# Kernel optimization log

Measured on AMD Instinct MI355X. Metric: run time of the kernel, lower is better.

Reference implementation:

```python
import jax, jax.numpy as jnp
import numpy as np

B, S, E, D, H, DH, FF, NL = 16384, 4, 1152, 192, 4, 48, 768, 2


def _ln(x, w, b, eps=1e-5):
    m = jnp.mean(x, axis=-1, keepdims=True)
    v = jnp.mean((x - m) ** 2, axis=-1, keepdims=True)
    return (x - m) * jax.lax.rsqrt(v + eps) * w + b


def _gelu(x):
    # torch nn.GELU / TransformerEncoderLayer(activation='gelu') use exact erf GELU
    return jax.nn.gelu(x, approximate=False)


def _pos_enc():
    pos = np.arange(S, dtype=np.float32)[:, None]
    div = np.exp(np.arange(0, D, 2, dtype=np.float32) * (-np.log(10000.0) / D))
    pe = np.zeros((S, D), dtype=np.float32)
    pe[:, 0::2] = np.sin(pos * div)
    pe[:, 1::2] = np.cos(pos * div)
    return jnp.asarray(pe)


def setup_inputs() -> dict:
    key = jax.random.key(0)
    ks = jax.random.split(key, 16)
    w = lambda k, shape: jax.random.normal(k, shape, jnp.float32) * 0.05
    return {
        'embeddings': jax.random.normal(ks[0], (B, S, E), jnp.float32),
        'in_ln_w': jnp.ones((E,), jnp.float32), 'in_ln_b': jnp.zeros((E,), jnp.float32),
        'in_proj_w': w(ks[1], (D, E)), 'in_proj_b': jnp.zeros((D,), jnp.float32),
        'qkv_w': w(ks[2], (NL, 3 * D, D)), 'qkv_b': jnp.zeros((NL, 3 * D), jnp.float32),
        'attn_out_w': w(ks[3], (NL, D, D)), 'attn_out_b': jnp.zeros((NL, D), jnp.float32),
        'ln1_w': jnp.ones((NL, D), jnp.float32), 'ln1_b': jnp.zeros((NL, D), jnp.float32),
        'ln2_w': jnp.ones((NL, D), jnp.float32), 'ln2_b': jnp.zeros((NL, D), jnp.float32),
        'ff1_w': w(ks[4], (NL, FF, D)), 'ff1_b': jnp.zeros((NL, FF), jnp.float32),
        'ff2_w': w(ks[5], (NL, D, FF)), 'ff2_b': jnp.zeros((NL, D), jnp.float32),
        'head_ln_w': jnp.ones((D,), jnp.float32), 'head_ln_b': jnp.zeros((D,), jnp.float32),
        'h1_w': w(ks[6], (256, D)), 'h1_b': jnp.zeros((256,), jnp.float32),
        'h2_w': w(ks[7], (64, 256)), 'h2_b': jnp.zeros((64,), jnp.float32),
        'h3_w': w(ks[8], (1, 64)) * 0.1, 'h3_b': jnp.zeros((1,), jnp.float32),
    }


def reference(embeddings, in_ln_w, in_ln_b, in_proj_w, in_proj_b,
              qkv_w, qkv_b, attn_out_w, attn_out_b,
              ln1_w, ln1_b, ln2_w, ln2_b,
              ff1_w, ff1_b, ff2_w, ff2_b,
              head_ln_w, head_ln_b, h1_w, h1_b, h2_w, h2_b, h3_w, h3_b):
    # input_proj: LN -> Linear(E, D) -> GELU (dropout is identity in eval)
    x = _ln(embeddings, in_ln_w, in_ln_b)
    x = _gelu(x @ in_proj_w.T + in_proj_b)
    # sinusoidal positional encoding
    x = x + _pos_enc()[None]
    scale = 1.0 / jnp.sqrt(jnp.float32(DH))
    # norm_first TransformerEncoder layers
    for i in range(NL):
        xn = _ln(x, ln1_w[i], ln1_b[i])
        qkv = xn @ qkv_w[i].T + qkv_b[i]                       # (B, S, 3D)
        q, k, v = jnp.split(qkv, 3, axis=-1)
        q = q.reshape(B, S, H, DH)
        k = k.reshape(B, S, H, DH)
        v = v.reshape(B, S, H, DH)
        scores = jnp.einsum('bqhd,bkhd->bhqk', q, k) * scale   # (B, H, S, S)
        attn = jax.nn.softmax(scores, axis=-1)
        o = jnp.einsum('bhqk,bkhd->bqhd', attn, v).reshape(B, S, D)
        x = x + (o @ attn_out_w[i].T + attn_out_b[i])
        xn = _ln(x, ln2_w[i], ln2_b[i])
        x = x + (_gelu(xn @ ff1_w[i].T + ff1_b[i]) @ ff2_w[i].T + ff2_b[i])
    pooled = x.mean(axis=1)                                    # (B, D)
    h = _ln(pooled, head_ln_w, head_ln_b)
    h = _gelu(h @ h1_w.T + h1_b)
    h = _gelu(h @ h2_w.T + h2_b)
    return (h @ h3_w.T + h3_b)[:, 0]                           # (B,)
```

## Files before the change

### kernel.cpp

```cpp
#include <hip/hip_runtime.h>
#include <hip/hip_bf16.h>
#include <math.h>

#define B_   16384
#define S_   4
#define E_   1152
#define D_   192
#define FF_  768
#define NL_  2
#define MTOK (B_ * S_)

typedef __attribute__((ext_vector_type(8))) _Float16 half8;
typedef __attribute__((ext_vector_type(4))) float floatx4;

__device__ __forceinline__ float gelu_f(float x) {
  return 0.5f * x * (1.0f + erff(x * 0.70710678118654752f));
}

__global__ __launch_bounds__(256) void cvt_f16_kernel(const float* __restrict__ s,
                                                      _Float16* __restrict__ d) {
  int i = (blockIdx.x * 256 + threadIdx.x) * 8;
  float4 a = *(const float4*)(s + i);
  float4 b = *(const float4*)(s + i + 4);
  half8 h;
  h[0] = (_Float16)a.x; h[1] = (_Float16)a.y; h[2] = (_Float16)a.z; h[3] = (_Float16)a.w;
  h[4] = (_Float16)b.x; h[5] = (_Float16)b.y; h[6] = (_Float16)b.z; h[7] = (_Float16)b.w;
  *(half8*)(d + i) = h;
}

__global__ __launch_bounds__(256) void prep_inproj_w(
    const float* __restrict__ W, const float* __restrict__ g,
    const float* __restrict__ b, const float* __restrict__ bias,
    _Float16* __restrict__ Wh, float* __restrict__ c1, float* __restrict__ c2) {
  const int n = blockIdx.x * 4 + (threadIdx.x >> 6);
  const int lane = threadIdx.x & 63;
  const float* Wr = W + (size_t)n * 1152;
  _Float16* Whr = Wh + (size_t)n * 1152;
  float s1 = 0.f, s2 = 0.f;
  #pragma unroll
  for (int j = 0; j < 18; ++j) {
    int k = lane + 64 * j;
    float wv = Wr[k];
    _Float16 h = (_Float16)(wv * g[k]);
    Whr[k] = h;
    s1 += (float)h;
    s2 = fmaf(b[k], wv, s2);
  }
  #pragma unroll
  for (int off = 1; off < 64; off <<= 1) {
    s1 += __shfl_xor(s1, off);
    s2 += __shfl_xor(s2, off);
  }
  if (lane == 0) { c1[n] = s1; c2[n] = s2 + bias[n]; }
}

__global__ __launch_bounds__(256) void inproj2_kernel(
    const float* __restrict__ emb, const _Float16* __restrict__ whp,
    const float* __restrict__ c1g, const float* __restrict__ c2g,
    float* __restrict__ xout, float* __restrict__ stD) {
  __shared__ __align__(16) _Float16 As[64][72];
  __shared__ float stats_[64][2];
  __shared__ float red_[4][64][2];
  __shared__ float pe_[4][192];
  const int tid = threadIdx.x;
  const int m0 = blockIdx.x * 64;
  const int w = tid >> 6, lane = tid & 63;
  const int ln16 = lane & 15, quad = lane >> 4;
  const int r_a = tid >> 2;
  const int c_a = (tid & 3) * 16;

  for (int i = tid; i < 768; i += 256) {
    int r = i / 192, col = i - r * 192;
    float ang = (float)r * expf((float)(col & ~1) * (-0.047970522770709292f));
    pe_[r][col] = (col & 1) ? cosf(ang) : sinf(ang);
  }

  const float* Arow = emb + (size_t)(m0 + r_a) * 1152 + c_a;
  const _Float16* wb = whp + (size_t)(w * 48 + ln16) * 1152 + quad * 8;

  float4 pa[4];
  auto loadA = [&](int k0) {
    #pragma unroll
    for (int j = 0; j < 4; ++j) pa[j] = *(const float4*)(Arow + k0 + j * 4);
  };

  float s = 0.f, q = 0.f;
  floatx4 acc[4][3] = {};
  loadA(0);
  for (int k0 = 0; k0 < 1152; k0 += 64) {
    __syncthreads();
    half8 h0, h1;
    h0[0] = (_Float16)pa[0].x; h0[1] = (_Float16)pa[0].y;
    h0[2] = (_Float16)pa[0].z; h0[3] = (_Float16)pa[0].w;
    h0[4] = (_Float16)pa[1].x; h0[5] = (_Float16)pa[1].y;
    h0[6] = (_Float16)pa[1].z; h0[7] = (_Float16)pa[1].w;
    h1[0] = (_Float16)pa[2].x; h1[1] = (_Float16)pa[2].y;
    h1[2] = (_Float16)pa[2].z; h1[3] = (_Float16)pa[2].w;
    h1[4] = (_Float16)pa[3].x; h1[5] = (_Float16)pa[3].y;
    h1[6] = (_Float16)pa[3].z; h1[7] = (_Float16)pa[3].w;
    *(half8*)&As[r_a][c_a] = h0;
    *(half8*)&As[r_a][c_a + 8] = h1;
    #pragma unroll
    for (int j = 0; j < 4; ++j) {
      s += pa[j].x + pa[j].y + pa[j].z + pa[j].w;
      q = fmaf(pa[j].x, pa[j].x, q); q = fmaf(pa[j].y, pa[j].y, q);
      q = fmaf(pa[j].z, pa[j].z, q); q = fmaf(pa[j].w, pa[j].w, q);
    }
    __syncthreads();
    if (k0 + 64 < 1152) loadA(k0 + 64);
    #pragma unroll
    for (int kk = 0; kk < 64; kk += 32) {
      half8 af[4], bf[3];
      #pragma unroll
      for (int mt = 0; mt < 4; ++mt)
        af[mt] = *(const half8*)&As[mt * 16 + ln16][kk + quad * 8];
      #pragma unroll
      for (int nt = 0; nt < 3; ++nt)
        bf[nt] = *(const half8*)(wb + (size_t)nt * 16 * 1152 + k0 + kk);
      #pragma unroll
      for (int mt = 0; mt < 4; ++mt)
        #pragma unroll
        for (int nt = 0; nt < 3; ++nt)
          acc[mt][nt] = __builtin_amdgcn_mfma_f32_16x16x32_f16(
              af[mt], bf[nt], acc[mt][nt], 0, 0, 0);
    }
  }

  s += __shfl_xor(s, 1); s += __shfl_xor(s, 2);
  q += __shfl_xor(q, 1); q += __shfl_xor(q, 2);
  if ((tid & 3) == 0) {
    float mean = s * (1.f / 1152.f);
    stats_[r_a][0] = mean;
    stats_[r_a][1] = rsqrtf(q * (1.f / 1152.f) - mean * mean + 1e-5f);
  }
  __syncthreads();

  float c1v[3], c2v[3];
  #pragma unroll
  for (int nt = 0; nt < 3; ++nt) {
    c1v[nt] = c1g[w * 48 + nt * 16 + ln16];
    c2v[nt] = c2g[w * 48 + nt * 16 + ln16];
  }
  float* xg = xout + (size_t)m0 * 192;
  #pragma unroll
  for (int mt = 0; mt < 4; ++mt) {
    #pragma unroll
    for (int r = 0; r < 4; ++r) {
      const int row = mt * 16 + quad * 4 + r;
      const float rm = stats_[row][0], rr = stats_[row][1];
      float so = 0.f, qo = 0.f;
      #pragma unroll
      for (int nt = 0; nt < 3; ++nt) {
        const int col = w * 48 + nt * 16 + ln16;
        float v = rr * (acc[mt][nt][r] - rm * c1v[nt]) + c2v[nt];
        v = gelu_f(v);
        v += pe_[r][col];
        xg[(size_t)row * 192 + col] = v;
        so += v;
        qo = fmaf(v, v, qo);
      }
      so += __shfl_xor(so, 1); so += __shfl_xor(so, 2);
      so += __shfl_xor(so, 4); so += __shfl_xor(so, 8);
      qo += __shfl_xor(qo, 1); qo += __shfl_xor(qo, 2);
      qo += __shfl_xor(qo, 4); qo += __shfl_xor(qo, 8);
      if (ln16 == 0) { red_[w][row][0] = so; red_[w][row][1] = qo; }
    }
  }
  __syncthreads();
  if (tid < 64) {
    float so = red_[0][tid][0] + red_[1][tid][0] + red_[2][tid][0] + red_[3][tid][0];
    float qo = red_[0][tid][1] + red_[1][tid][1] + red_[2][tid][1] + red_[3][tid][1];
    float mean = so * (1.f / 192.f);
    stD[2 * (m0 + tid)] = mean;
    stD[2 * (m0 + tid) + 1] = rsqrtf(qo * (1.f / 192.f) - mean * mean + 1e-5f);
  }
}

__global__ __launch_bounds__(256) void layer_attn_kernel(
    float* __restrict__ x, const _Float16* __restrict__ wqkv,
    const float* __restrict__ bqkv, const _Float16* __restrict__ wao,
    const float* __restrict__ bao, const float* __restrict__ ln1g,
    const float* __restrict__ ln1b_, float* __restrict__ stD) {
  __shared__ __align__(16) _Float16 xh[32][200];
  __shared__ __align__(16) _Float16 qk[32][584];
  __shared__ float sp[8][4][4][4];
  const int tid = threadIdx.x;
  const int m0 = blockIdx.x * 32;
  const int w = tid >> 6, lane = tid & 63;
  const int ln16 = lane & 15, quad = lane >> 4;

  {
    const int ra = tid >> 3, ca = (tid & 7) * 24;
    const float sm = stD[2 * (m0 + ra)], srs = stD[2 * (m0 + ra) + 1];
    const float* Ar = x + (size_t)(m0 + ra) * 192 + ca;
    #pragma unroll
    for (int j = 0; j < 3; ++j) {
      float4 a0 = *(const float4*)(Ar + j * 8);
      float4 a1 = *(const float4*)(Ar + j * 8 + 4);
      float4 g0 = *(const float4*)(ln1g + ca + j * 8);
      float4 g1 = *(const float4*)(ln1g + ca + j * 8 + 4);
      float4 b0 = *(const float4*)(ln1b_ + ca + j * 8);
      float4 b1 = *(const float4*)(ln1b_ + ca + j * 8 + 4);
      half8 h;
      h[0] = (_Float16)((a0.x - sm) * srs * g0.x + b0.x);
      h[1] = (_Float16)((a0.y - sm) * srs * g0.y + b0.y);
      h[2] = (_Float16)((a0.z - sm) * srs * g0.z + b0.z);
      h[3] = (_Float16)((a0.w - sm) * srs * g0.w + b0.w);
      h[4] = (_Float16)((a1.x - sm) * srs * g1.x + b1.x);
      h[5] = (_Float16)((a1.y - sm) * srs * g1.y + b1.y);
      h[6] = (_Float16)((a1.z - sm) * srs * g1.z + b1.z);
      h[7] = (_Float16)((a1.w - sm) * srs * g1.w + b1.w);
      *(half8*)&xh[ra][ca + j * 8] = h;
    }
  }
  __syncthreads();

  for (int nt = 0; nt < 9; ++nt) {
    const int nc = w * 144 + nt * 16;
    half8 bf[6];
    const _Float16* wp = wqkv + (size_t)(nc + ln16) * 192 + quad * 8;
    #pragma unroll
    for (int k = 0; k < 6; ++k) bf[k] = *(const half8*)(wp + k * 32);
    floatx4 a0v = {}, a1v = {};
    #pragma unroll
    for (int k = 0; k < 6; ++k) {
      half8 f0 = *(const half8*)&xh[ln16][k * 32 + quad * 8];
      half8 f1 = *(const half8*)&xh[16 + ln16][k * 32 + quad * 8];
      a0v = __builtin_amdgcn_mfma_f32_16x16x32_f16(f0, bf[k], a0v, 0, 0, 0);
      a1v = __builtin_amdgcn_mfma_f32_16x16x32_f16(f1, bf[k], a1v, 0, 0, 0);
    }
    const float bv = bqkv[nc + ln16];
    #pragma unroll
    for (int r = 0; r < 4; ++r) {
      qk[quad * 4 + r][nc + ln16]      = (_Float16)(a0v[r] + bv);
      qk[16 + quad * 4 + r][nc + ln16] = (_Float16)(a1v[r] + bv);
    }
  }
  __syncthreads();

  #pragma unroll
  for (int s2 = 0; s2 < 2; ++s2) {
    const int sg = w * 2 + s2;
    const int h = lane >> 4, i = (lane >> 2) & 3, j = lane & 3;
    const _Float16* qp = &qk[4 * sg + i][h * 48];
    const _Float16* kp = &qk[4 * sg + j][192 + h * 48];
    float s = 0.f;
    #pragma unroll
    for (int d = 0; d < 6; ++d) {
      half8 qv = *(const half8*)(qp + d * 8);
      half8 kv = *(const half8*)(kp + d * 8);
      #pragma unroll
      for (int e = 0; e < 8; ++e) s += (float)qv[e] * (float)kv[e];
    }
    s *= 0.14433756729740643f;
    float mx = fmaxf(s, __shfl_xor(s, 1));
    mx = fmaxf(mx, __shfl_xor(mx, 2));
    float e = expf(s - mx);
    float sum = e + __shfl_xor(e, 1);
    sum += __shfl_xor(sum, 2);
    sp[sg][h][i][j] = e / sum;
  }
  #pragma unroll
  for (int s2 = 0; s2 < 2; ++s2) {
    const int sg = w * 2 + s2;
    #pragma unroll
    for (int ii = 0; ii < 4; ++ii) {
      #pragma unroll
      for (int cc = 0; cc < 3; ++cc) {
        const int c = lane + cc * 64;
        const int hh = c / 48;
        float a = 0.f;
        #pragma unroll
        for (int jj = 0; jj < 4; ++jj)
          a += sp[sg][hh][ii][jj] * (float)qk[4 * sg + jj][384 + c];
        xh[4 * sg + ii][c] = (_Float16)a;
      }
    }
  }
  __syncthreads();

  float* outs = (float*)&qk[0][0];
  #pragma unroll
  for (int nt = 0; nt < 3; ++nt) {
    const int nc = w * 48 + nt * 16;
    half8 bf[6];
    const _Float16* wp = wao + (size_t)(nc + ln16) * 192 + quad * 8;
    #pragma unroll
    for (int k = 0; k < 6; ++k) bf[k] = *(const half8*)(wp + k * 32);
    floatx4 a0v = {}, a1v = {};
    #pragma unroll
    for (int k = 0; k < 6; ++k) {
      half8 f0 = *(const half8*)&xh[ln16][k * 32 + quad * 8];
      half8 f1 = *(const half8*)&xh[16 + ln16][k * 32 + quad * 8];
      a0v = __builtin_amdgcn_mfma_f32_16x16x32_f16(f0, bf[k], a0v, 0, 0, 0);
      a1v = __builtin_amdgcn_mfma_f32_16x16x32_f16(f1, bf[k], a1v, 0, 0, 0);
    }
    const float bv = bao[nc + ln16];
    #pragma unroll
    for (int r = 0; r < 4; ++r) {
      outs[(quad * 4 + r) * 192 + nc + ln16]      = a0v[r] + bv;
      outs[(16 + quad * 4 + r) * 192 + nc + ln16] = a1v[r] + bv;
    }
  }
  __syncthreads();

  {
    const int fbase = tid * 6;
    const int row = tid >> 3;
    float* xg = x + (size_t)m0 * 192;
    float s = 0.f, q = 0.f;
    #pragma unroll
    for (int j = 0; j < 6; ++j) {
      float4 v = ((const float4*)outs)[fbase + j];
      float4 rr = *(const float4*)(xg + (fbase + j) * 4);
      v.x += rr.x; v.y += rr.y; v.z += rr.z; v.w += rr.w;
      s += v.x + v.y + v.z + v.w;
      q += v.x * v.x + v.y * v.y + v.z * v.z + v.w * v.w;
      *(float4*)(xg + (fbase + j) * 4) = v;
    }
    s += __shfl_xor(s, 1); s += __shfl_xor(s, 2); s += __shfl_xor(s, 4);
    q += __shfl_xor(q, 1); q += __shfl_xor(q, 2); q += __shfl_xor(q, 4);
    if ((tid & 7) == 0) {
      float mean = s * (1.f / 192.f);
      stD[2 * (m0 + row)] = mean;
      stD[2 * (m0 + row) + 1] = rsqrtf(q * (1.f / 192.f) - mean * mean + 1e-5f);
    }
  }
}

__global__ __launch_bounds__(256) void layer_ff_kernel(
    float* __restrict__ x, const _Float16* __restrict__ wff1,
    const float* __restrict__ bff1, const _Float16* __restrict__ wff2,
    const float* __restrict__ bff2, const float* __restrict__ ln2g,
    const float* __restrict__ ln2b_, float* __restrict__ stD) {
  __shared__ __align__(16) char pool[51200];
  _Float16 (*xh2)[200] = (_Float16 (*)[200])pool;
  _Float16 (*ffh)[200] = (_Float16 (*)[200])(pool + 25600);
  const int tid = threadIdx.x;
  const int m0 = blockIdx.x * 64;
  const int w = tid >> 6, lane = tid & 63;
  const int ln16 = lane & 15, quad = lane >> 4;

  {
    const int ra = tid >> 2, ca = (tid & 3) * 48;
    const float sm = stD[2 * (m0 + ra)], srs = stD[2 * (m0 + ra) + 1];
    const float* Ar = x + (size_t)(m0 + ra) * 192 + ca;
    #pragma unroll
    for (int j = 0; j < 6; ++j) {
      float4 a0 = *(const float4*)(Ar + j * 8);
      float4 a1 = *(const float4*)(Ar + j * 8 + 4);
      float4 g0 = *(const float4*)(ln2g + ca + j * 8);
      float4 g1 = *(const float4*)(ln2g + ca + j * 8 + 4);
      float4 b0 = *(const float4*)(ln2b_ + ca + j * 8);
      float4 b1 = *(const float4*)(ln2b_ + ca + j * 8 + 4);
      half8 h;
      h[0] = (_Float16)((a0.x - sm) * srs * g0.x + b0.x);
      h[1] = (_Float16)((a0.y - sm) * srs * g0.y + b0.y);
      h[2] = (_Float16)((a0.z - sm) * srs * g0.z + b0.z);
      h[3] = (_Float16)((a0.w - sm) * srs * g0.w + b0.w);
      h[4] = (_Float16)((a1.x - sm) * srs * g1.x + b1.x);
      h[5] = (_Float16)((a1.y - sm) * srs * g1.y + b1.y);
      h[6] = (_Float16)((a1.z - sm) * srs * g1.z + b1.z);
      h[7] = (_Float16)((a1.w - sm) * srs * g1.w + b1.w);
      *(half8*)&xh2[ra][ca + j * 8] = h;
    }
  }
  __syncthreads();

  floatx4 acc2[4][3] = {};
  for (int qq = 0; qq < 4; ++qq) {
    #pragma unroll
    for (int nt = 0; nt < 3; ++nt) {
      const int ng = qq * 192 + w * 48 + nt * 16;
      const int nl = w * 48 + nt * 16;
      half8 bf[6];
      const _Float16* wp = wff1 + (size_t)(ng + ln16) * 192 + quad * 8;
      #pragma unroll
      for (int k = 0; k < 6; ++k) bf[k] = *(const half8*)(wp + k * 32);
      floatx4 a4[4] = {};
      #pragma unroll
      for (int k = 0; k < 6; ++k) {
        #pragma unroll
        for (int mt = 0; mt < 4; ++mt) {
          half8 af = *(const half8*)&xh2[mt * 16 + ln16][k * 32 + quad * 8];
          a4[mt] = __builtin_amdgcn_mfma_f32_16x16x32_f16(af, bf[k], a4[mt], 0, 0, 0);
        }
      }
      const float bv = bff1[ng + ln16];
      #pragma unroll
      for (int mt = 0; mt < 4; ++mt)
        #pragma unroll
        for (int r = 0; r < 4; ++r)
          ffh[mt * 16 + quad * 4 + r][nl + ln16] = (_Float16)gelu_f(a4[mt][r] + bv);
    }
    __syncthreads();
    for (int k12 = 0; k12 < 6; ++k12) {
      half8 af[4];
      #pragma unroll
      for (int mt = 0; mt < 4; ++mt)
        af[mt] = *(const half8*)&ffh[mt * 16 + ln16][k12 * 32 + quad * 8];
      #pragma unroll
      for (int nt = 0; nt < 3; ++nt) {
        const int nc = w * 48 + nt * 16;
        half8 bf = *(const half8*)(wff2 + (size_t)(nc + ln16) * 768 +
                                   qq * 192 + k12 * 32 + quad * 8);
        #pragma unroll
        for (int mt = 0; mt < 4; ++mt)
          acc2[mt][nt] = __builtin_amdgcn_mfma_f32_16x16x32_f16(
              af[mt], bf, acc2[mt][nt], 0, 0, 0);
      }
    }
    __syncthreads();
  }

  float* outs = (float*)pool;
  #pragma unroll
  for (int nt = 0; nt < 3; ++nt) {
    const int nc = w * 48 + nt * 16;
    const float bv = bff2[nc + ln16];
    #pragma unroll
    for (int mt = 0; mt < 4; ++mt)
      #pragma unroll
      for (int r = 0; r < 4; ++r)
        outs[(mt * 16 + quad * 4 + r) * 192 + nc + ln16] = acc2[mt][nt][r] + bv;
  }
  __syncthreads();

  {
    const int fbase = tid * 12;
    const int row = tid >> 2;
    float* xg = x + (size_t)m0 * 192;
    float s = 0.f, q = 0.f;
    #pragma unroll
    for (int j = 0; j < 12; ++j) {
      float4 v = ((const float4*)outs)[fbase + j];
      float4 rr = *(const float4*)(xg + (fbase + j) * 4);
      v.x += rr.x; v.y += rr.y; v.z += rr.z; v.w += rr.w;
      s += v.x + v.y + v.z + v.w;
      q += v.x * v.x + v.y * v.y + v.z * v.z + v.w * v.w;
      *(float4*)(xg + (fbase + j) * 4) = v;
    }
    s += __shfl_xor(s, 1); s += __shfl_xor(s, 2);
    q += __shfl_xor(q, 1); q += __shfl_xor(q, 2);
    if ((tid & 3) == 0) {
      float mean = s * (1.f / 192.f);
      stD[2 * (m0 + row)] = mean;
      stD[2 * (m0 + row) + 1] = rsqrtf(q * (1.f / 192.f) - mean * mean + 1e-5f);
    }
  }
}

template <int EPI>
__global__ __launch_bounds__(256) void gemm_f32(
    const float* __restrict__ A, const float* __restrict__ W,
    const float* __restrict__ bias, float* __restrict__ C,
    int M, int N, int K) {
  __shared__ float As[16][68];
  __shared__ float Bs[16][68];
  const int tid = threadIdx.x;
  const int m0 = blockIdx.x * 64;
  const int n0 = blockIdx.y * 64;
  const int tx = tid & 15, ty = tid >> 4;
  const int lr = tid >> 2;
  const int lk = (tid & 3) << 2;
  float acc[4][4] = {};
  const float* Arow = A + (size_t)(m0 + lr) * K;
  const float* Wrow = W + (size_t)(n0 + lr) * K;
  for (int k0 = 0; k0 < K; k0 += 16) {
    float4 av = *(const float4*)(Arow + k0 + lk);
    float4 wv = *(const float4*)(Wrow + k0 + lk);
    __syncthreads();
    As[lk + 0][lr] = av.x; As[lk + 1][lr] = av.y;
    As[lk + 2][lr] = av.z; As[lk + 3][lr] = av.w;
    Bs[lk + 0][lr] = wv.x; Bs[lk + 1][lr] = wv.y;
    Bs[lk + 2][lr] = wv.z; Bs[lk + 3][lr] = wv.w;
    __syncthreads();
    #pragma unroll
    for (int kk = 0; kk < 16; ++kk) {
      float4 a = *(const float4*)&As[kk][ty * 4];
      float4 b = *(const float4*)&Bs[kk][tx * 4];
      acc[0][0] += a.x * b.x; acc[0][1] += a.x * b.y; acc[0][2] += a.x * b.z; acc[0][3] += a.x * b.w;
      acc[1][0] += a.y * b.x; acc[1][1] += a.y * b.y; acc[1][2] += a.y * b.z; acc[1][3] += a.y * b.w;
      acc[2][0] += a.z * b.x; acc[2][1] += a.z * b.y; acc[2][2] += a.z * b.z; acc[2][3] += a.z * b.w;
      acc[3][0] += a.w * b.x; acc[3][1] += a.w * b.y; acc[3][2] += a.w * b.z; acc[3][3] += a.w * b.w;
    }
  }
  float4 bv = *(const float4*)(bias + n0 + tx * 4);
  #pragma unroll
  for (int i = 0; i < 4; ++i) {
    int m = m0 + ty * 4 + i;
    float v0 = acc[i][0] + bv.x, v1 = acc[i][1] + bv.y;
    float v2 = acc[i][2] + bv.z, v3 = acc[i][3] + bv.w;
    if constexpr (EPI == 1) {
      v0 = gelu_f(v0); v1 = gelu_f(v1); v2 = gelu_f(v2); v3 = gelu_f(v3);
    }
    float4 ov; ov.x = v0; ov.y = v1; ov.z = v2; ov.w = v3;
    *(float4*)(C + (size_t)m * N + n0 + tx * 4) = ov;
  }
}

__global__ __launch_bounds__(256) void pool_ln_kernel(const float* __restrict__ x,
                                                      const float* __restrict__ g,
                                                      const float* __restrict__ b,
                                                      float* __restrict__ hout) {
  int bi = blockIdx.x * 4 + (threadIdx.x >> 6);
  int lane = threadIdx.x & 63;
  const float* row = x + (size_t)bi * 4 * D_;
  float vals[3];
  float sum = 0.f;
  #pragma unroll
  for (int cc = 0; cc < 3; ++cc) {
    int d = lane + cc * 64;
    float v = 0.25f * (row[d] + row[D_ + d] + row[2 * D_ + d] + row[3 * D_ + d]);
    vals[cc] = v; sum += v;
  }
  #pragma unroll
  for (int off = 1; off < 64; off <<= 1) sum += __shfl_xor(sum, off);
  float mean = sum / (float)D_;
  float vs = 0.f;
  #pragma unroll
  for (int cc = 0; cc < 3; ++cc) { float d0 = vals[cc] - mean; vs += d0 * d0; }
  #pragma unroll
  for (int off = 1; off < 64; off <<= 1) vs += __shfl_xor(vs, off);
  float rstd = rsqrtf(vs / (float)D_ + 1e-5f);
  #pragma unroll
  for (int cc = 0; cc < 3; ++cc) {
    int d = lane + cc * 64;
    hout[(size_t)bi * D_ + d] = (vals[cc] - mean) * rstd * g[d] + b[d];
  }
}

__global__ __launch_bounds__(256) void head_final_kernel(const float* __restrict__ h2,
                                                         const float* __restrict__ w,
                                                         const float* __restrict__ b,
                                                         float* __restrict__ out) {
  int bi = blockIdx.x * 4 + (threadIdx.x >> 6);
  int lane = threadIdx.x & 63;
  float v = h2[(size_t)bi * 64 + lane] * w[lane];
  #pragma unroll
  for (int off = 1; off < 64; off <<= 1) v += __shfl_xor(v, off);
  if (lane == 0) out[bi] = v + b[0];
}

extern "C" void kernel_launch(void* const* d_in, const int* in_sizes, int n_in,
                              void* d_out, int out_size, void* d_ws, size_t ws_size,
                              hipStream_t stream) {
  (void)in_sizes; (void)n_in; (void)out_size; (void)ws_size;
  const float* emb       = (const float*)d_in[0];
  const float* in_ln_w   = (const float*)d_in[1];
  const float* in_ln_b   = (const float*)d_in[2];
  const float* in_proj_w = (const float*)d_in[3];
  const float* in_proj_b = (const float*)d_in[4];
  const float* qkv_w     = (const float*)d_in[5];
  const float* qkv_b     = (const float*)d_in[6];
  const float* aow       = (const float*)d_in[7];
  const float* aob       = (const float*)d_in[8];
  const float* ln1w      = (const float*)d_in[9];
  const float* ln1b      = (const float*)d_in[10];
  const float* ln2w      = (const float*)d_in[11];
  const float* ln2b      = (const float*)d_in[12];
  const float* ff1w      = (const float*)d_in[13];
  const float* ff1b      = (const float*)d_in[14];
  const float* ff2w      = (const float*)d_in[15];
  const float* ff2b      = (const float*)d_in[16];
  const float* hlnw      = (const float*)d_in[17];
  const float* hlnb      = (const float*)d_in[18];
  const float* h1w       = (const float*)d_in[19];
  const float* h1b       = (const float*)d_in[20];
  const float* h2w       = (const float*)d_in[21];
  const float* h2b       = (const float*)d_in[22];
  const float* h3w       = (const float*)d_in[23];
  const float* h3b       = (const float*)d_in[24];
  float* out = (float*)d_out;

  float* ws = (float*)d_ws;
  size_t off = 0;
  float* x   = ws + off; off += (size_t)MTOK * D_;
  float* stD = ws + off; off += (size_t)MTOK * 2;
  float* hp  = ws + off; off += (size_t)B_ * D_;
  float* h1  = ws + off; off += (size_t)B_ * 256;
  float* h2  = ws + off; off += (size_t)B_ * 64;
  float* c1  = ws + off; off += 192;
  float* c2  = ws + off; off += 192;
  _Float16* wh = (_Float16*)(ws + off);
  _Float16* w_inproj = wh;
  _Float16* w_qkv    = w_inproj + 221184;
  _Float16* w_ao     = w_qkv    + 221184;
  _Float16* w_ff1    = w_ao     + 73728;
  _Float16* w_ff2    = w_ff1    + 294912;

  prep_inproj_w<<<48, 256, 0, stream>>>(in_proj_w, in_ln_w, in_ln_b, in_proj_b,
                                        w_inproj, c1, c2);
  cvt_f16_kernel<<<221184 / 2048, 256, 0, stream>>>(qkv_w, w_qkv);
  cvt_f16_kernel<<<73728  / 2048, 256, 0, stream>>>(aow, w_ao);
  cvt_f16_kernel<<<294912 / 2048, 256, 0, stream>>>(ff1w, w_ff1);
  cvt_f16_kernel<<<294912 / 2048, 256, 0, stream>>>(ff2w, w_ff2);

  inproj2_kernel<<<MTOK / 64, 256, 0, stream>>>(emb, w_inproj, c1, c2, x, stD);

  for (int i = 0; i < NL_; ++i) {
    layer_attn_kernel<<<MTOK / 32, 256, 0, stream>>>(
        x, w_qkv + (size_t)i * 110592, qkv_b + (size_t)i * 576,
        w_ao + (size_t)i * 36864, aob + (size_t)i * 192,
        ln1w + (size_t)i * 192, ln1b + (size_t)i * 192, stD);
    layer_ff_kernel<<<MTOK / 64, 256, 0, stream>>>(
        x, w_ff1 + (size_t)i * 147456, ff1b + (size_t)i * 768,
        w_ff2 + (size_t)i * 147456, ff2b + (size_t)i * 192,
        ln2w + (size_t)i * 192, ln2b + (size_t)i * 192, stD);
  }

  pool_ln_kernel<<<B_ / 4, 256, 0, stream>>>(x, hlnw, hlnb, hp);
  gemm_f32<1><<<dim3(B_ / 64, 256 / 64), 256, 0, stream>>>(hp, h1w, h1b, h1, B_, 256, D_);
  gemm_f32<1><<<dim3(B_ / 64, 64 / 64), 256, 0, stream>>>(h1, h2w, h2b, h2, B_, 64, 256);
  head_final_kernel<<<B_ / 4, 256, 0, stream>>>(h2, h3w, h3b, out);
}
```

Before: 998.5 us.

## Fuse pooling, head LayerNorm and MLP head into one MFMA fp16 kernel

Replaces the four head kernels (pool+LN, two fp32 SIMT GEMMs with GELU, final dot) with a single kernel that pools eight samples per block, normalizes, and runs both head GEMMs with fp16 MFMA, keeping intermediates in shared memory. Head weights are converted to fp16 up front. This removes the global round-trips for the pooled, h1 and h2 buffers and the slow scalar fp32 GEMMs. In exchange, half of each 16-row MFMA tile is padding, and fp16 precision is used in the head.

Result: faster. 973.9 us (-2.5%).

```diff
diff --git a/kernel.cpp b/kernel.cpp
--- a/kernel.cpp
+++ b/kernel.cpp
@@ -450,96 +450,107 @@
   }
 }
 
-template <int EPI>
-__global__ __launch_bounds__(256) void gemm_f32(
-    const float* __restrict__ A, const float* __restrict__ W,
-    const float* __restrict__ bias, float* __restrict__ C,
-    int M, int N, int K) {
-  __shared__ float As[16][68];
-  __shared__ float Bs[16][68];
+__global__ __launch_bounds__(256) void head_kernel(
+    const float* __restrict__ x,
+    const float* __restrict__ hlng, const float* __restrict__ hlnb,
+    const _Float16* __restrict__ h1wh, const float* __restrict__ h1b,
+    const _Float16* __restrict__ h2wh, const float* __restrict__ h2b,
+    const float* __restrict__ h3w, const float* __restrict__ h3b,
+    float* __restrict__ out) {
+  __shared__ __align__(16) _Float16 ph[16][200];
+  __shared__ __align__(16) char pool[24576];
   const int tid = threadIdx.x;
-  const int m0 = blockIdx.x * 64;
-  const int n0 = blockIdx.y * 64;
-  const int tx = tid & 15, ty = tid >> 4;
-  const int lr = tid >> 2;
-  const int lk = (tid & 3) << 2;
-  float acc[4][4] = {};
-  const float* Arow = A + (size_t)(m0 + lr) * K;
-  const float* Wrow = W + (size_t)(n0 + lr) * K;
-  for (int k0 = 0; k0 < K; k0 += 16) {
-    float4 av = *(const float4*)(Arow + k0 + lk);
-    float4 wv = *(const float4*)(Wrow + k0 + lk);
-    __syncthreads();
-    As[lk + 0][lr] = av.x; As[lk + 1][lr] = av.y;
-    As[lk + 2][lr] = av.z; As[lk + 3][lr] = av.w;
-    Bs[lk + 0][lr] = wv.x; Bs[lk + 1][lr] = wv.y;
-    Bs[lk + 2][lr] = wv.z; Bs[lk + 3][lr] = wv.w;
-    __syncthreads();
-    #pragma unroll
-    for (int kk = 0; kk < 16; ++kk) {
-      float4 a = *(const float4*)&As[kk][ty * 4];
-      float4 b = *(const float4*)&Bs[kk][tx * 4];
-      acc[0][0] += a.x * b.x; acc[0][1] += a.x * b.y; acc[0][2] += a.x * b.z; acc[0][3] += a.x * b.w;
-      acc[1][0] += a.y * b.x; acc[1][1] += a.y * b.y; acc[1][2] += a.y * b.z; acc[1][3] += a.y * b.w;
-      acc[2][0] += a.z * b.x; acc[2][1] += a.z * b.y; acc[2][2] += a.z * b.z; acc[2][3] += a.z * b.w;
-      acc[3][0] += a.w * b.x; acc[3][1] += a.w * b.y; acc[3][2] += a.w * b.z; acc[3][3] += a.w * b.w;
-    }
-  }
-  float4 bv = *(const float4*)(bias + n0 + tx * 4);
-  #pragma unroll
-  for (int i = 0; i < 4; ++i) {
-    int m = m0 + ty * 4 + i;
-    float v0 = acc[i][0] + bv.x, v1 = acc[i][1] + bv.y;
-    float v2 = acc[i][2] + bv.z, v3 = acc[i][3] + bv.w;
-    if constexpr (EPI == 1) {
-      v0 = gelu_f(v0); v1 = gelu_f(v1); v2 = gelu_f(v2); v3 = gelu_f(v3);
-    }
-    float4 ov; ov.x = v0; ov.y = v1; ov.z = v2; ov.w = v3;
-    *(float4*)(C + (size_t)m * N + n0 + tx * 4) = ov;
-  }
-}
-
-__global__ __launch_bounds__(256) void pool_ln_kernel(const float* __restrict__ x,
-                                                      const float* __restrict__ g,
-                                                      const float* __restrict__ b,
-                                                      float* __restrict__ hout) {
-  int bi = blockIdx.x * 4 + (threadIdx.x >> 6);
-  int lane = threadIdx.x & 63;
-  const float* row = x + (size_t)bi * 4 * D_;
-  float vals[3];
-  float sum = 0.f;
-  #pragma unroll
-  for (int cc = 0; cc < 3; ++cc) {
-    int d = lane + cc * 64;
-    float v = 0.25f * (row[d] + row[D_ + d] + row[2 * D_ + d] + row[3 * D_ + d]);
-    vals[cc] = v; sum += v;
-  }
-  #pragma unroll
-  for (int off = 1; off < 64; off <<= 1) sum += __shfl_xor(sum, off);
-  float mean = sum / (float)D_;
-  float vs = 0.f;
-  #pragma unroll
-  for (int cc = 0; cc < 3; ++cc) { float d0 = vals[cc] - mean; vs += d0 * d0; }
-  #pragma unroll
-  for (int off = 1; off < 64; off <<= 1) vs += __shfl_xor(vs, off);
-  float rstd = rsqrtf(vs / (float)D_ + 1e-5f);
-  #pragma unroll
-  for (int cc = 0; cc < 3; ++cc) {
-    int d = lane + cc * 64;
-    hout[(size_t)bi * D_ + d] = (vals[cc] - mean) * rstd * g[d] + b[d];
-  }
-}
-
-__global__ __launch_bounds__(256) void head_final_kernel(const float* __restrict__ h2,
-                                                         const float* __restrict__ w,
-                                                         const float* __restrict__ b,
-                                                         float* __restrict__ out) {
-  int bi = blockIdx.x * 4 + (threadIdx.x >> 6);
-  int lane = threadIdx.x & 63;
-  float v = h2[(size_t)bi * 64 + lane] * w[lane];
-  #pragma unroll
-  for (int off = 1; off < 64; off <<= 1) v += __shfl_xor(v, off);
-  if (lane == 0) out[bi] = v + b[0];
+  const int m0 = blockIdx.x * 32;
+  const int w = tid >> 6, lane = tid & 63;
+  const int ln16 = lane & 15, quad = lane >> 4;
+
+  {
+    float* xs = (float*)pool;
+    const int fbase = tid * 6;
+    const float* xg = x + (size_t)m0 * 192;
+    #pragma unroll
+    for (int j = 0; j < 6; ++j)
+      *(float4*)(xs + (fbase + j) * 4) = *(const float4*)(xg + (fbase + j) * 4);
+  }
+  __syncthreads();
+
+  {
+    const float* xs = (const float*)pool;
+    const int s = tid >> 5, u = tid & 31;
+    float pv[6];
+    float ss = 0.f, qq = 0.f;
+    #pragma unroll
+    for (int c6 = 0; c6 < 6; ++c6) {
+      const int c = u * 6 + c6;
+      float v = 0.25f * (xs[(4 * s) * 192 + c] + xs[(4 * s + 1) * 192 + c] +
+                         xs[(4 * s + 2) * 192 + c] + xs[(4 * s + 3) * 192 + c]);
+      pv[c6] = v; ss += v; qq = fmaf(v, v, qq);
+    }
+    ss += __shfl_xor(ss, 1); ss += __shfl_xor(ss, 2); ss += __shfl_xor(ss, 4);
+    ss += __shfl_xor(ss, 8); ss += __shfl_xor(ss, 16);
+    qq += __shfl_xor(qq, 1); qq += __shfl_xor(qq, 2); qq += __shfl_xor(qq, 4);
+    qq += __shfl_xor(qq, 8); qq += __shfl_xor(qq, 16);
+    const float mean = ss * (1.f / 192.f);
+    const float rs = rsqrtf(qq * (1.f / 192.f) - mean * mean + 1e-5f);
+    #pragma unroll
+    for (int c6 = 0; c6 < 6; ++c6) {
+      const int c = u * 6 + c6;
+      ph[s][c] = (_Float16)((pv[c6] - mean) * rs * hlng[c] + hlnb[c]);
+      ph[8 + s][c] = (_Float16)0.f;
+    }
+  }
+  __syncthreads();
+
+  _Float16 (*h1s)[264] = (_Float16 (*)[264])pool;
+  #pragma unroll
+  for (int nt = 0; nt < 4; ++nt) {
+    const int nc = w * 64 + nt * 16;
+    half8 bf[6];
+    const _Float16* wp = h1wh + (size_t)(nc + ln16) * 192 + quad * 8;
+    #pragma unroll
+    for (int k = 0; k < 6; ++k) bf[k] = *(const half8*)(wp + k * 32);
+    floatx4 a4 = {};
+    #pragma unroll
+    for (int k = 0; k < 6; ++k) {
+      half8 af = *(const half8*)&ph[ln16][k * 32 + quad * 8];
+      a4 = __builtin_amdgcn_mfma_f32_16x16x32_f16(af, bf[k], a4, 0, 0, 0);
+    }
+    const float bv = h1b[nc + ln16];
+    #pragma unroll
+    for (int r = 0; r < 4; ++r) {
+      const int rr = quad * 4 + r;
+      h1s[rr][nc + ln16] = (rr < 8) ? (_Float16)gelu_f(a4[r] + bv) : (_Float16)0.f;
+    }
+  }
+  __syncthreads();
+
+  _Float16 (*h2s)[72] = (_Float16 (*)[72])(pool + 16384);
+  {
+    const int nc = w * 16;
+    floatx4 a4 = {};
+    #pragma unroll
+    for (int k = 0; k < 8; ++k) {
+      half8 af = *(const half8*)&h1s[ln16][k * 32 + quad * 8];
+      half8 bf = *(const half8*)(h2wh + (size_t)(nc + ln16) * 256 + k * 32 + quad * 8);
+      a4 = __builtin_amdgcn_mfma_f32_16x16x32_f16(af, bf, a4, 0, 0, 0);
+    }
+    const float bv = h2b[nc + ln16];
+    #pragma unroll
+    for (int r = 0; r < 4; ++r) {
+      const int rr = quad * 4 + r;
+      if (rr < 8) h2s[rr][nc + ln16] = (_Float16)gelu_f(a4[r] + bv);
+    }
+  }
+  __syncthreads();
+
+  {
+    const int s = tid >> 5, u = tid & 31;
+    float v = (float)h2s[s][2 * u] * h3w[2 * u] +
+              (float)h2s[s][2 * u + 1] * h3w[2 * u + 1];
+    v += __shfl_xor(v, 1); v += __shfl_xor(v, 2); v += __shfl_xor(v, 4);
+    v += __shfl_xor(v, 8); v += __shfl_xor(v, 16);
+    if (u == 0) out[blockIdx.x * 8 + s] = v + h3b[0];
+  }
 }
 
 extern "C" void kernel_launch(void* const* d_in, const int* in_sizes, int n_in,
@@ -577,9 +588,6 @@
   size_t off = 0;
   float* x   = ws + off; off += (size_t)MTOK * D_;
   float* stD = ws + off; off += (size_t)MTOK * 2;
-  float* hp  = ws + off; off += (size_t)B_ * D_;
-  float* h1  = ws + off; off += (size_t)B_ * 256;
-  float* h2  = ws + off; off += (size_t)B_ * 64;
   float* c1  = ws + off; off += 192;
   float* c2  = ws + off; off += 192;
   _Float16* wh = (_Float16*)(ws + off);
@@ -588,6 +596,8 @@
   _Float16* w_ao     = w_qkv    + 221184;
   _Float16* w_ff1    = w_ao     + 73728;
   _Float16* w_ff2    = w_ff1    + 294912;
+  _Float16* w_h1     = w_ff2    + 294912;
+  _Float16* w_h2     = w_h1     + 49152;
 
   prep_inproj_w<<<48, 256, 0, stream>>>(in_proj_w, in_ln_w, in_ln_b, in_proj_b,
                                         w_inproj, c1, c2);
@@ -595,6 +605,8 @@
   cvt_f16_kernel<<<73728  / 2048, 256, 0, stream>>>(aow, w_ao);
   cvt_f16_kernel<<<294912 / 2048, 256, 0, stream>>>(ff1w, w_ff1);
   cvt_f16_kernel<<<294912 / 2048, 256, 0, stream>>>(ff2w, w_ff2);
+  cvt_f16_kernel<<<49152  / 2048, 256, 0, stream>>>(h1w, w_h1);
+  cvt_f16_kernel<<<16384  / 2048, 256, 0, stream>>>(h2w, w_h2);
 
   inproj2_kernel<<<MTOK / 64, 256, 0, stream>>>(emb, w_inproj, c1, c2, x, stD);
 
@@ -609,8 +621,6 @@
         ln2w + (size_t)i * 192, ln2b + (size_t)i * 192, stD);
   }
 
-  pool_ln_kernel<<<B_ / 4, 256, 0, stream>>>(x, hlnw, hlnb, hp);
-  gemm_f32<1><<<dim3(B_ / 64, 256 / 64), 256, 0, stream>>>(hp, h1w, h1b, h1, B_, 256, D_);
-  gemm_f32<1><<<dim3(B_ / 64, 64 / 64), 256, 0, stream>>>(h1, h2w, h2b, h2, B_, 64, 256);
-  head_final_kernel<<<B_ / 4, 256, 0, stream>>>(h2, h3w, h3b, out);
-}
+  head_kernel<<<MTOK / 32, 256, 0, stream>>>(
+      x, hlnw, hlnb, w_h1, h1b, w_h2, h2b, h3w, h3b, out);
+}
```
